# Kernel optimization log

Hardware: AMD Instinct MI355X
Metric: run time of the kernel (lower is better)

Reference implementation:

```python
import jax, jax.numpy as jnp
import numpy as np

H = 16
D_MODEL = 1024
D_K = D_MODEL // H
L = 4096


def setup_inputs() -> dict:
    key = jax.random.key(0)
    ks = jax.random.split(key, 11)
    s = 1.0 / np.sqrt(D_MODEL)
    inp = {
        "query": jax.random.normal(ks[0], (L, D_MODEL), dtype=jnp.float32),
        "key": jax.random.normal(ks[1], (L, D_MODEL), dtype=jnp.float32),
        "value": jax.random.normal(ks[2], (L, D_MODEL), dtype=jnp.float32),
        "Wq": jax.random.uniform(ks[3], (D_MODEL, D_MODEL), jnp.float32, -s, s),
        "Wk": jax.random.uniform(ks[4], (D_MODEL, D_MODEL), jnp.float32, -s, s),
        "Wv": jax.random.uniform(ks[5], (D_MODEL, D_MODEL), jnp.float32, -s, s),
        "Wo": jax.random.uniform(ks[6], (D_MODEL, D_MODEL), jnp.float32, -s, s),
        "bq": jax.random.uniform(ks[7], (D_MODEL,), jnp.float32, -s, s),
        "bk": jax.random.uniform(ks[8], (D_MODEL,), jnp.float32, -s, s),
        "bv": jax.random.uniform(ks[9], (D_MODEL,), jnp.float32, -s, s),
        "bo": jax.random.uniform(ks[10], (D_MODEL,), jnp.float32, -s, s),
    }
    return inp


def reference(query, key, value, Wq, Wk, Wv, Wo, bq, bk, bv, bo):
    # projections: torch Linear computes x @ W.T + b
    def proj(x, W, b):
        # [L, d_model] -> [h, L, d_k]
        y = x @ W.T + b
        return y.reshape(L, H, D_K).transpose(1, 0, 2)

    q = proj(query, Wq, bq)   # [h, L, d_k]
    k = proj(key, Wk, bk)
    v = proj(value, Wv, bv)

    scores = jnp.einsum("hqd,hkd->hqk", q, k) / jnp.sqrt(jnp.float32(D_K))  # [h, L, L]
    p = jax.nn.softmax(scores, axis=-1)
    x = jnp.einsum("hqk,hkd->hqd", p, v)         # [h, L, d_k]
    x = x.transpose(1, 0, 2).reshape(L, H * D_K)  # [L, d_model]
    return x @ Wo.T + bo
```

## Files before the change

kernel.cpp:

```cpp
#include <hip/hip_runtime.h>

#define L_SEQ 4096
#define DM 1024
#define NH 16
#define DK 64

typedef short s16x8 __attribute__((ext_vector_type(8)));
typedef float f32x4 __attribute__((ext_vector_type(4)));
typedef float f32x16 __attribute__((ext_vector_type(16)));
typedef unsigned u32x2 __attribute__((ext_vector_type(2)));
typedef unsigned short u16t;
typedef unsigned int u32t;

typedef __attribute__((address_space(1))) unsigned int as1_u32;
typedef __attribute__((address_space(3))) unsigned int as3_u32;

#define GLOAD_LDS16(gsrc, ldst) \
  __builtin_amdgcn_global_load_lds((as1_u32*)(gsrc), (as3_u32*)(ldst), 16, 0, 0)

__device__ __forceinline__ u16t f2bf(float f) {
  union { float f; unsigned u; } v; v.f = f;
  unsigned u = v.u;
  u += 0x7fffu + ((u >> 16) & 1u);
  return (u16t)(u >> 16);
}

__device__ __forceinline__ float fexp2(float x) {
  float r;
  asm("v_exp_f32 %0, %1" : "=v"(r) : "v"(x));
  return r;
}

__device__ __forceinline__ float max3f(float a, float b, float c) {
  return fmaxf(fmaxf(a, b), c);
}

struct CvtArgs { const float* s[7]; u16t* d[7]; };

__global__ __launch_bounds__(256) void cvt_all(CvtArgs a) {
  int g = blockIdx.x * 256 + threadIdx.x;
  int seg, off;
  if (g < 1572864) { seg = g >> 19;               off = g & 524287; }
  else             { int t = g - 1572864; seg = 3 + (t >> 17); off = t & 131071; }
  const float* src = a.s[seg] + (size_t)off * 8;
  u16t* dst = a.d[seg] + (size_t)off * 8;
  float4 x = *(const float4*)(src);
  float4 y = *(const float4*)(src + 4);
  uint4 o;
  o.x = (u32t)f2bf(x.x) | ((u32t)f2bf(x.y) << 16);
  o.y = (u32t)f2bf(x.z) | ((u32t)f2bf(x.w) << 16);
  o.z = (u32t)f2bf(y.x) | ((u32t)f2bf(y.y) << 16);
  o.w = (u32t)f2bf(y.z) | ((u32t)f2bf(y.w) << 16);
  *(uint4*)dst = o;
}

struct QkvArgs {
  const u16t* A[3]; const u16t* Bm[3]; const float* bias[3]; u16t* C[3];
  float scale0;
};

__global__ __launch_bounds__(256)
void gemm_qkv(QkvArgs ga) {
  __shared__ unsigned char lds[2][2][8192];
  const int bid = blockIdx.x;
  const int z = bid >> 8;
  const int b = bid & 255;
  const int bc = (z == 2) ? (b & 31) : (b & 7);
  const int br = (z == 2) ? (b >> 5) : (b >> 3);
  const int N  = (z == 2) ? L_SEQ : DM;
  const float osc = (z == 0) ? ga.scale0 : 1.0f;
  const bool rowb = (z == 2);
  const u16t* A = ga.A[z];
  const u16t* Bm = ga.Bm[z];
  const float* bias = ga.bias[z];
  u16t* C = ga.C[z];
  const int K = DM;

  const int tid = threadIdx.x;
  const int lane = tid & 63;
  const int wv = tid >> 6;
  const int wr = wv >> 1, wc = wv & 1;
  const int l15 = lane & 15, l4 = lane >> 4;

  const int r_st = tid >> 2;
  const int c_st = (tid & 3) ^ ((r_st >> 1) & 3);
  const u16t* a0 = A + (size_t)(br * 128 + r_st) * K + c_st * 8;
  const u16t* a1 = a0 + (size_t)64 * K;
  const u16t* b0 = Bm + (size_t)(bc * 128 + r_st) * K + c_st * 8;
  const u16t* b1 = b0 + (size_t)64 * K;
  const int woff = wv * 1024;

  f32x4 acc[4][4] = {};

  auto stage = [&](int buf, int k0) {
    GLOAD_LDS16(a0 + k0, &lds[buf][0][woff]);
    GLOAD_LDS16(a1 + k0, &lds[buf][0][4096 + woff]);
    GLOAD_LDS16(b0 + k0, &lds[buf][1][woff]);
    GLOAD_LDS16(b1 + k0, &lds[buf][1][4096 + woff]);
  };

  const int nt = K >> 5;
  stage(0, 0);
  int buf = 0;
  for (int t = 0; t < nt; ++t) {
    __syncthreads();
    if (t + 1 < nt) stage(buf ^ 1, (t + 1) * 32);
    s16x8 af[4], bfr[4];
    #pragma unroll
    for (int m = 0; m < 4; ++m) {
      int r = wr * 64 + m * 16 + l15;
      int sl = l4 ^ ((r >> 1) & 3);
      af[m] = *(const s16x8*)&lds[buf][0][r * 64 + (sl << 4)];
    }
    #pragma unroll
    for (int n = 0; n < 4; ++n) {
      int r = wc * 64 + n * 16 + l15;
      int sl = l4 ^ ((r >> 1) & 3);
      bfr[n] = *(const s16x8*)&lds[buf][1][r * 64 + (sl << 4)];
    }
    #pragma unroll
    for (int m = 0; m < 4; ++m)
      #pragma unroll
      for (int n = 0; n < 4; ++n)
        acc[m][n] = __builtin_amdgcn_mfma_f32_16x16x32_bf16(af[m], bfr[n], acc[m][n], 0, 0, 0);
    buf ^= 1;
  }

  #pragma unroll
  for (int m = 0; m < 4; ++m) {
    #pragma unroll
    for (int n = 0; n < 4; ++n) {
      #pragma unroll
      for (int i = 0; i < 4; ++i) {
        int row = br * 128 + wr * 64 + m * 16 + l4 * 4 + i;
        int col = bc * 128 + wc * 64 + n * 16 + l15;
        float v = (acc[m][n][i] + (rowb ? bias[row] : bias[col])) * osc;
        C[(size_t)row * N + col] = f2bf(v);
      }
    }
  }
}

__global__ __launch_bounds__(256)
void gemm_out(const u16t* __restrict__ A, const u16t* __restrict__ B,
              const float* __restrict__ bias, float* __restrict__ C,
              int M, int N, int K) {
  __shared__ unsigned char lds[2][12288];
  const int tid = threadIdx.x;
  const int lane = tid & 63;
  const int wv = tid >> 6;
  const int wr = wv >> 1, wc = wv & 1;
  const int l15 = lane & 15, l4 = lane >> 4;
  const int bc = blockIdx.x, br = blockIdx.y;

  const int r_st = tid >> 2;
  const int c_st = (tid & 3) ^ ((r_st >> 1) & 3);
  const u16t* a0 = A + (size_t)(br * 128 + r_st) * K + c_st * 8;
  const u16t* a1 = a0 + (size_t)64 * K;
  const u16t* b0 = B + (size_t)(bc * 64 + r_st) * K + c_st * 8;
  const int woff = wv * 1024;

  f32x4 acc[4][2] = {};

  auto stage = [&](int buf, int k0) {
    GLOAD_LDS16(a0 + k0, &lds[buf][woff]);
    GLOAD_LDS16(a1 + k0, &lds[buf][4096 + woff]);
    GLOAD_LDS16(b0 + k0, &lds[buf][8192 + woff]);
  };

  const int nt = K >> 5;
  stage(0, 0);
  int buf = 0;
  for (int t = 0; t < nt; ++t) {
    __syncthreads();
    if (t + 1 < nt) stage(buf ^ 1, (t + 1) * 32);
    s16x8 af[4], bfr[2];
    #pragma unroll
    for (int m = 0; m < 4; ++m) {
      int r = wr * 64 + m * 16 + l15;
      int sl = l4 ^ ((r >> 1) & 3);
      af[m] = *(const s16x8*)&lds[buf][r * 64 + (sl << 4)];
    }
    #pragma unroll
    for (int n = 0; n < 2; ++n) {
      int r = wc * 32 + n * 16 + l15;
      int sl = l4 ^ ((r >> 1) & 3);
      bfr[n] = *(const s16x8*)&lds[buf][8192 + r * 64 + (sl << 4)];
    }
    #pragma unroll
    for (int m = 0; m < 4; ++m)
      #pragma unroll
      for (int n = 0; n < 2; ++n)
        acc[m][n] = __builtin_amdgcn_mfma_f32_16x16x32_bf16(af[m], bfr[n], acc[m][n], 0, 0, 0);
    buf ^= 1;
  }

  #pragma unroll
  for (int m = 0; m < 4; ++m) {
    #pragma unroll
    for (int n = 0; n < 2; ++n) {
      #pragma unroll
      for (int i = 0; i < 4; ++i) {
        int row = br * 128 + wr * 64 + m * 16 + l4 * 4 + i;
        int col = bc * 64 + wc * 32 + n * 16 + l15;
        C[(size_t)row * N + col] = acc[m][n][i] + bias[col];
      }
    }
  }
}

#define PKBF(dst, a, b) \
  asm("v_cvt_pk_bf16_f32 %0, %1, %2" : "=v"(dst) : "v"(a), "v"(b))

#define MAKE_FRAG(S, B, FR) { \
    u32t w0, w1, w2, w3; \
    PKBF(w0, S[B + 0], S[B + 1]); PKBF(w1, S[B + 2], S[B + 3]); \
    PKBF(w2, S[B + 4], S[B + 5]); PKBF(w3, S[B + 6], S[B + 7]); \
    u32x2 r02 = __builtin_amdgcn_permlane32_swap(w0, w2, false, false); \
    u32x2 r13 = __builtin_amdgcn_permlane32_swap(w1, w3, false, false); \
    union { u32t u[4]; s16x8 v; } uu; \
    uu.u[0] = r02[0]; uu.u[1] = r13[0]; uu.u[2] = r02[1]; uu.u[3] = r13[1]; \
    FR = uu.v; }

__global__ __launch_bounds__(512, 2)
void attn_fused(const u16t* __restrict__ Qp, const u16t* __restrict__ Kp,
                const u16t* __restrict__ VpT, u16t* __restrict__ AO) {
  __shared__ unsigned char sStage[3][16384];

  const int tid = threadIdx.x;
  const int lane = tid & 63;
  const int w = tid >> 6;
  const int l31 = lane & 31;
  const int hi = lane >> 5;
  const int h = blockIdx.y;
  const int qrow = blockIdx.x * 256 + w * 32 + l31;

  s16x8 qf[4];
  {
    const u16t* qsrc = Qp + (size_t)qrow * DM + h * DK + hi * 8;
    #pragma unroll
    for (int c = 0; c < 4; ++c) qf[c] = *(const s16x8*)(qsrc + c * 16);
  }

  f32x16 acc0 = {}, acc1 = {};
  float mrow = -3.0e38f, lrow = 0.f;

  auto stage = [&](int buf, int kv) {
    GLOAD_LDS16(Kp + (size_t)(kv + lane) * DM + h * DK + w * 8,
                &sStage[buf][w * 1024]);
    GLOAD_LDS16(VpT + (size_t)(h * DK + lane) * L_SEQ + kv + w * 8,
                &sStage[buf][8192 + w * 1024]);
  };

  auto compute = [&](const unsigned char* sb) {
    f32x16 st0 = {}, st1 = {};
    __builtin_amdgcn_s_setprio(1);
    #pragma unroll
    for (int c = 0; c < 4; ++c) {
      const unsigned char* kp = sb + (((c * 2 + hi) << 10));
      s16x8 kf0 = *(const s16x8*)(kp + (l31 << 4));
      s16x8 kf1 = *(const s16x8*)(kp + ((32 + l31) << 4));
      st0 = __builtin_amdgcn_mfma_f32_32x32x16_bf16(kf0, qf[c], st0, 0, 0, 0);
      st1 = __builtin_amdgcn_mfma_f32_32x32x16_bf16(kf1, qf[c], st1, 0, 0, 0);
    }
    __builtin_amdgcn_s_setprio(0);

    float v0 = max3f(st0[0], st0[1], st0[2]);
    float v1 = max3f(st0[3], st0[4], st0[5]);
    float v2 = max3f(st0[6], st0[7], st0[8]);
    float v3 = max3f(st0[9], st0[10], st0[11]);
    float v4 = max3f(st0[12], st0[13], st0[14]);
    float v5 = max3f(st1[0], st1[1], st1[2]);
    float v6 = max3f(st1[3], st1[4], st1[5]);
    float v7 = max3f(st1[6], st1[7], st1[8]);
    float v8 = max3f(st1[9], st1[10], st1[11]);
    float v9 = max3f(st1[12], st1[13], st1[14]);
    float va = fmaxf(st0[15], st1[15]);
    float mx = max3f(max3f(v0, v1, v2), max3f(v3, v4, v5),
                     max3f(max3f(v6, v7, v8), v9, va));
    mx = fmaxf(mx, __shfl_xor(mx, 32));

    float mnew = fmaxf(mrow, mx);
    if (!__all(mx <= mrow)) {
      float alpha = fexp2(mrow - mnew);
      lrow *= alpha;
      #pragma unroll
      for (int r = 0; r < 16; ++r) { acc0[r] *= alpha; acc1[r] *= alpha; }
      mrow = mnew;
    }
    const float m2 = mrow;

    #pragma unroll
    for (int r = 0; r < 16; ++r) {
      st0[r] = fexp2(st0[r] - m2);
      st1[r] = fexp2(st1[r] - m2);
    }
    float s8[8];
    #pragma unroll
    for (int r = 0; r < 8; ++r)
      s8[r] = (st0[2*r] + st0[2*r+1]) + (st1[2*r] + st1[2*r+1]);
    float rs = ((s8[0] + s8[1]) + (s8[2] + s8[3])) +
               ((s8[4] + s8[5]) + (s8[6] + s8[7]));
    rs += __shfl_xor(rs, 32);
    lrow += rs;

    __builtin_amdgcn_s_setprio(1);
    #pragma unroll
    for (int cc = 0; cc < 4; ++cc) {
      s16x8 pfr;
      if (cc == 0)      MAKE_FRAG(st0, 0, pfr)
      else if (cc == 1) MAKE_FRAG(st0, 8, pfr)
      else if (cc == 2) MAKE_FRAG(st1, 0, pfr)
      else              MAKE_FRAG(st1, 8, pfr)
      const unsigned char* vp = sb + 8192 + ((cc * 2 + hi) << 10);
      s16x8 vf0 = *(const s16x8*)(vp + (l31 << 4));
      s16x8 vf1 = *(const s16x8*)(vp + ((32 + l31) << 4));
      acc0 = __builtin_amdgcn_mfma_f32_32x32x16_bf16(vf0, pfr, acc0, 0, 0, 0);
      acc1 = __builtin_amdgcn_mfma_f32_32x32x16_bf16(vf1, pfr, acc1, 0, 0, 0);
    }
    __builtin_amdgcn_s_setprio(0);
  };

  stage(0, 0);
  stage(1, 64);
  int cur = 0, nstage = 2;
  for (int t = 0; t < 63; ++t) {
    asm volatile("s_waitcnt vmcnt(2)" ::: "memory");
    __builtin_amdgcn_s_barrier();
    __builtin_amdgcn_sched_barrier(0);
    if (t < 62) {
      stage(nstage, (t + 2) * 64);
      nstage = (nstage == 2) ? 0 : nstage + 1;
    }
    compute(sStage[cur]);
    cur = (cur == 2) ? 0 : cur + 1;
  }
  asm volatile("s_waitcnt vmcnt(0)" ::: "memory");
  __builtin_amdgcn_s_barrier();
  __builtin_amdgcn_sched_barrier(0);
  compute(sStage[cur]);

  const float inv = 1.0f / lrow;
  u16t* orow = AO + (size_t)qrow * DM + h * DK;
  #pragma unroll
  for (int r = 0; r < 16; ++r) {
    int d = (r & 3) + 8 * (r >> 2) + 4 * hi;
    orow[d]      = f2bf(acc0[r] * inv);
    orow[32 + d] = f2bf(acc1[r] * inv);
  }
}

extern "C" void kernel_launch(void* const* d_in, const int* in_sizes, int n_in,
                              void* d_out, int out_size, void* d_ws, size_t ws_size,
                              hipStream_t stream) {
  const float* query = (const float*)d_in[0];
  const float* key_  = (const float*)d_in[1];
  const float* value = (const float*)d_in[2];
  const float* Wq = (const float*)d_in[3];
  const float* Wk = (const float*)d_in[4];
  const float* Wv = (const float*)d_in[5];
  const float* Wo = (const float*)d_in[6];
  const float* bq = (const float*)d_in[7];
  const float* bk = (const float*)d_in[8];
  const float* bv = (const float*)d_in[9];
  const float* bo = (const float*)d_in[10];

  char* ws = (char*)d_ws;
  const size_t MB = 1u << 20;
  u16t* qb  = (u16t*)(ws + 0 * MB);
  u16t* kb  = (u16t*)(ws + 8 * MB);
  u16t* vb  = (u16t*)(ws + 16 * MB);
  u16t* wqb = (u16t*)(ws + 24 * MB);
  u16t* wkb = (u16t*)(ws + 26 * MB);
  u16t* wvb = (u16t*)(ws + 28 * MB);
  u16t* wob = (u16t*)(ws + 30 * MB);
  u16t* Qp  = (u16t*)(ws + 32 * MB);
  u16t* Kp  = (u16t*)(ws + 40 * MB);
  u16t* VpT = (u16t*)(ws + 48 * MB);
  u16t* AO  = (u16t*)(ws + 56 * MB);

  const float QSCALE = 0.125f * 1.4426950408889634f;

  CvtArgs ca;
  ca.s[0] = query; ca.s[1] = key_; ca.s[2] = value;
  ca.s[3] = Wq; ca.s[4] = Wk; ca.s[5] = Wv; ca.s[6] = Wo;
  ca.d[0] = qb; ca.d[1] = kb; ca.d[2] = vb;
  ca.d[3] = wqb; ca.d[4] = wkb; ca.d[5] = wvb; ca.d[6] = wob;
  cvt_all<<<dim3(8192), dim3(256), 0, stream>>>(ca);

  QkvArgs ga;
  ga.A[0] = qb;  ga.Bm[0] = wqb; ga.bias[0] = bq; ga.C[0] = Qp;
  ga.A[1] = kb;  ga.Bm[1] = wkb; ga.bias[1] = bk; ga.C[1] = Kp;
  ga.A[2] = wvb; ga.Bm[2] = vb;  ga.bias[2] = bv; ga.C[2] = VpT;
  ga.scale0 = QSCALE;
  gemm_qkv<<<dim3(768), dim3(256), 0, stream>>>(ga);

  attn_fused<<<dim3(L_SEQ / 256, NH), dim3(512), 0, stream>>>(Qp, Kp, VpT, AO);

  gemm_out<<<dim3(DM / 64, L_SEQ / 128), dim3(256), 0, stream>>>(
      AO, wob, bo, (float*)d_out, L_SEQ, DM, DM);
}
```

Baseline: 163.4 us.

## Split attention KV range in two and merge partials with combine kernel

Splits the attention kernel's key/value sequence into two halves along a new grid z dimension, so each block writes an unnormalized partial output plus its row max and sum. A new combine kernel rescales and merges the two partials into the final attention output. Launch bounds are raised to allow more blocks per CU. The original grid had only 256 blocks, so this doubles parallelism to fill the GPU. The cost is an extra launch, extra global traffic for the partials, and a second bf16 rounding of the unnormalized partials.

```diff
diff --git a/kernel.cpp b/kernel.cpp
--- a/kernel.cpp
+++ b/kernel.cpp
@@ -33,6 +33,13 @@
 
 __device__ __forceinline__ float max3f(float a, float b, float c) {
   return fmaxf(fmaxf(a, b), c);
+}
+
+__device__ __forceinline__ float bflo(u32t u) {
+  union { u32t u; float f; } v; v.u = u << 16; return v.f;
+}
+__device__ __forceinline__ float bfhi(u32t u) {
+  union { u32t u; float f; } v; v.u = u & 0xffff0000u; return v.f;
 }
 
 struct CvtArgs { const float* s[7]; u16t* d[7]; };
@@ -222,9 +229,11 @@
     uu.u[0] = r02[0]; uu.u[1] = r13[0]; uu.u[2] = r02[1]; uu.u[3] = r13[1]; \
     FR = uu.v; }
 
-__global__ __launch_bounds__(512, 2)
+__global__ __launch_bounds__(512, 4)
 void attn_fused(const u16t* __restrict__ Qp, const u16t* __restrict__ Kp,
-                const u16t* __restrict__ VpT, u16t* __restrict__ AO) {
+                const u16t* __restrict__ VpT, u16t* __restrict__ Op0,
+                u16t* __restrict__ Op1, float2* __restrict__ Ml0,
+                float2* __restrict__ Ml1) {
   __shared__ unsigned char sStage[3][16384];
 
   const int tid = threadIdx.x;
@@ -233,7 +242,11 @@
   const int l31 = lane & 31;
   const int hi = lane >> 5;
   const int h = blockIdx.y;
+  const int z = blockIdx.z;
+  const int kvbase = z * (L_SEQ / 2);
   const int qrow = blockIdx.x * 256 + w * 32 + l31;
+  u16t* Opz = z ? Op1 : Op0;
+  float2* Mlz = z ? Ml1 : Ml0;
 
   s16x8 qf[4];
   {
@@ -321,15 +334,15 @@
     __builtin_amdgcn_s_setprio(0);
   };
 
-  stage(0, 0);
-  stage(1, 64);
+  stage(0, kvbase);
+  stage(1, kvbase + 64);
   int cur = 0, nstage = 2;
-  for (int t = 0; t < 63; ++t) {
+  for (int t = 0; t < 31; ++t) {
     asm volatile("s_waitcnt vmcnt(2)" ::: "memory");
     __builtin_amdgcn_s_barrier();
     __builtin_amdgcn_sched_barrier(0);
-    if (t < 62) {
-      stage(nstage, (t + 2) * 64);
+    if (t < 30) {
+      stage(nstage, kvbase + (t + 2) * 64);
       nstage = (nstage == 2) ? 0 : nstage + 1;
     }
     compute(sStage[cur]);
@@ -340,14 +353,54 @@
   __builtin_amdgcn_sched_barrier(0);
   compute(sStage[cur]);
 
-  const float inv = 1.0f / lrow;
-  u16t* orow = AO + (size_t)qrow * DM + h * DK;
+  u16t* orow = Opz + (size_t)qrow * DM + h * DK;
   #pragma unroll
-  for (int r = 0; r < 16; ++r) {
-    int d = (r & 3) + 8 * (r >> 2) + 4 * hi;
-    orow[d]      = f2bf(acc0[r] * inv);
-    orow[32 + d] = f2bf(acc1[r] * inv);
-  }
+  for (int rq = 0; rq < 4; ++rq) {
+    union { u16t h4[4]; uint2 v; } p0, p1;
+    #pragma unroll
+    for (int i = 0; i < 4; ++i) {
+      p0.h4[i] = f2bf(acc0[4 * rq + i]);
+      p1.h4[i] = f2bf(acc1[4 * rq + i]);
+    }
+    int d0 = 8 * rq + 4 * hi;
+    *(uint2*)(orow + d0)      = p0.v;
+    *(uint2*)(orow + 32 + d0) = p1.v;
+  }
+  if (hi == 0) Mlz[h * L_SEQ + qrow] = make_float2(mrow, lrow);
+}
+
+__global__ __launch_bounds__(256)
+void attn_combine(const u16t* __restrict__ O0, const u16t* __restrict__ O1,
+                  const float2* __restrict__ Ml0, const float2* __restrict__ Ml1,
+                  u16t* __restrict__ AO) {
+  int g = blockIdx.x * 256 + threadIdx.x;
+  int qh = g >> 2;
+  int d0 = (g & 3) * 16;
+  int q = qh >> 4, h = qh & 15;
+  size_t off = (size_t)q * DM + h * DK + d0;
+
+  float2 ml0 = Ml0[h * L_SEQ + q];
+  float2 ml1 = Ml1[h * L_SEQ + q];
+  float m = fmaxf(ml0.x, ml1.x);
+  float w0 = fexp2(ml0.x - m), w1 = fexp2(ml1.x - m);
+  float inv = 1.0f / (ml0.y * w0 + ml1.y * w1);
+  float s0 = w0 * inv, s1 = w1 * inv;
+
+  uint4 a[2], b[2], o[2];
+  a[0] = *(const uint4*)(O0 + off);     a[1] = *(const uint4*)(O0 + off + 8);
+  b[0] = *(const uint4*)(O1 + off);     b[1] = *(const uint4*)(O1 + off + 8);
+  #pragma unroll
+  for (int k = 0; k < 2; ++k) {
+    u32t* au = (u32t*)&a[k]; u32t* bu = (u32t*)&b[k]; u32t* ou = (u32t*)&o[k];
+    #pragma unroll
+    for (int j = 0; j < 4; ++j) {
+      float lo = bflo(au[j]) * s0 + bflo(bu[j]) * s1;
+      float hf = bfhi(au[j]) * s0 + bfhi(bu[j]) * s1;
+      ou[j] = (u32t)f2bf(lo) | ((u32t)f2bf(hf) << 16);
+    }
+  }
+  *(uint4*)(AO + off)     = o[0];
+  *(uint4*)(AO + off + 8) = o[1];
 }
 
 extern "C" void kernel_launch(void* const* d_in, const int* in_sizes, int n_in,
@@ -379,6 +432,11 @@
   u16t* VpT = (u16t*)(ws + 48 * MB);
   u16t* AO  = (u16t*)(ws + 56 * MB);
 
+  u16t* Op0   = (u16t*)(ws + 0 * MB);
+  u16t* Op1   = (u16t*)(ws + 8 * MB);
+  float2* Ml0 = (float2*)(ws + 16 * MB);
+  float2* Ml1 = (float2*)(ws + 17 * MB);
+
   const float QSCALE = 0.125f * 1.4426950408889634f;
 
   CvtArgs ca;
@@ -395,7 +453,10 @@
   ga.scale0 = QSCALE;
   gemm_qkv<<<dim3(768), dim3(256), 0, stream>>>(ga);
 
-  attn_fused<<<dim3(L_SEQ / 256, NH), dim3(512), 0, stream>>>(Qp, Kp, VpT, AO);
+  attn_fused<<<dim3(L_SEQ / 256, NH, 2), dim3(512), 0, stream>>>(
+      Qp, Kp, VpT, Op0, Op1, Ml0, Ml1);
+
+  attn_combine<<<dim3(1024), dim3(256), 0, stream>>>(Op0, Op1, Ml0, Ml1, AO);
 
   gemm_out<<<dim3(DM / 64, L_SEQ / 128), dim3(256), 0, stream>>>(
       AO, wob, bo, (float*)d_out, L_SEQ, DM, DM);
```

Result: slower. 169.4 us (+3.7%).
